# Kernel tuning notes

Hardware: AMD Instinct MI355X
Metric: run time of the kernel (lower is better)

Reference implementation:

```python
import jax, jax.numpy as jnp
import numpy as np

NUM_ORGAN = 13
EPS = 1e-05


def setup_inputs() -> dict:
    key = jax.random.key(0)
    k1, k2, k3 = jax.random.split(key, 3)
    B = 2
    pred_stage1 = jax.random.uniform(k1, (B, NUM_ORGAN + 1, 48, 256, 256), dtype=jnp.float32)
    pred_stage2 = jax.random.uniform(k2, (B, NUM_ORGAN + 1, 48, 256, 256), dtype=jnp.float32)
    target = jax.random.randint(k3, (B, 48, 256, 256), 0, NUM_ORGAN + 1, dtype=jnp.int32)
    return {"pred_stage1": pred_stage1, "pred_stage2": pred_stage2, "target": target}


def _dice_per_batch(pred, organ_target):
    # pred: (B, 14, D, H, W); organ_target: (B, 13, D, H, W) one-hot
    p = pred[:, 1:NUM_ORGAN + 1]                       # (B, 13, D, H, W)
    inter = jnp.sum(p * organ_target, axis=(2, 3, 4))  # (B, 13)
    p2 = jnp.sum(p * p, axis=(2, 3, 4))                # (B, 13)
    t2 = jnp.sum(organ_target, axis=(2, 3, 4))         # one-hot => t^2 == t
    dice = 2.0 * inter / (p2 + t2 + EPS)               # (B, 13)
    return jnp.sum(dice, axis=1) / NUM_ORGAN           # (B,)


def reference(pred_stage1, pred_stage2, target):
    organ_ids = jnp.arange(1, NUM_ORGAN + 1, dtype=target.dtype)
    # one-hot over organ classes 1..13 -> (B, 13, D, H, W)
    organ_target = (target[:, None] == organ_ids[None, :, None, None, None]).astype(pred_stage1.dtype)
    dice = _dice_per_batch(pred_stage1, organ_target) + _dice_per_batch(pred_stage2, organ_target)
    return jnp.mean(2.0 - dice)
```

## Files before the change

### kernel.cpp

```cpp
#include <hip/hip_runtime.h>

#define NORG 13
#define NCH  14
#define VOX  (48 * 256 * 256)
#define EPSF 1e-5f
#define CHUNK 8192
#define NCHUNK (VOX / CHUNK)
#define ITER (CHUNK / 4 / 256)
#define COMBO_STRIDE 16

__device__ __forceinline__ float wave_reduce(float v) {
#pragma unroll
    for (int off = 32; off; off >>= 1) v += __shfl_xor(v, off, 64);
    return v;
}

__global__ __launch_bounds__(256) void dice_partial(
    const float* __restrict__ pred1, const float* __restrict__ pred2,
    const int* __restrict__ tgt, float* __restrict__ acc_out)
{
    const int b     = blockIdx.y;
    const int chunk = blockIdx.x;
    const size_t v0 = (size_t)chunk * CHUNK;

    __shared__ unsigned char t_lds[CHUNK];
    __shared__ float acc[NORG * 5];

    if (threadIdx.x < NORG * 5) acc[threadIdx.x] = 0.f;

    const int4* tb = (const int4*)(tgt + (size_t)b * VOX + v0);
    uchar4* tl4 = (uchar4*)t_lds;
#pragma unroll
    for (int i = 0; i < ITER; ++i) {
        const int4 t = tb[i * 256 + threadIdx.x];
        tl4[i * 256 + threadIdx.x] =
            make_uchar4((unsigned char)t.x, (unsigned char)t.y,
                        (unsigned char)t.z, (unsigned char)t.w);
    }
    __syncthreads();

    const uchar4* tl = (const uchar4*)t_lds;
    const int lane = threadIdx.x & 63;

    for (int o = 0; o < NORG; ++o) {
        const int ch = o + 1;
        const float4* p1 = (const float4*)(pred1 + ((size_t)b * NCH + ch) * VOX + v0);
        const float4* p2 = (const float4*)(pred2 + ((size_t)b * NCH + ch) * VOX + v0);

        float i1 = 0.f, s1 = 0.f, i2 = 0.f, s2 = 0.f, cn = 0.f;
#pragma unroll
        for (int i = 0; i < ITER; ++i) {
            const int idx = i * 256 + threadIdx.x;
            const uchar4 t = tl[idx];
            const float4 a = p1[idx];
            const float4 c = p2[idx];
            const float m0 = (t.x == ch) ? 1.f : 0.f;
            const float m1 = (t.y == ch) ? 1.f : 0.f;
            const float m2 = (t.z == ch) ? 1.f : 0.f;
            const float m3 = (t.w == ch) ? 1.f : 0.f;
            s1 += a.x * a.x + a.y * a.y + a.z * a.z + a.w * a.w;
            s2 += c.x * c.x + c.y * c.y + c.z * c.z + c.w * c.w;
            i1 += m0 * a.x + m1 * a.y + m2 * a.z + m3 * a.w;
            i2 += m0 * c.x + m1 * c.y + m2 * c.z + m3 * c.w;
            cn += (m0 + m1) + (m2 + m3);
        }

        float vals[5] = {i1, s1, i2, s2, cn};
#pragma unroll
        for (int s = 0; s < 5; ++s) {
            const float r = wave_reduce(vals[s]);
            if (lane == 0) atomicAdd(&acc[o * 5 + s], r);
        }
    }

    __syncthreads();
    if (threadIdx.x < NORG * 5) {
        const int o = threadIdx.x / 5;
        const int s = threadIdx.x % 5;
        atomicAdd(&acc_out[(b * NORG + o) * COMBO_STRIDE + s], acc[threadIdx.x]);
    }
}

__global__ void dice_final(const float* __restrict__ acc,
                           float* __restrict__ out, int B)
{
    if (threadIdx.x == 0 && blockIdx.x == 0) {
        float total = 0.f;
        for (int b = 0; b < B; ++b) {
            float d1 = 0.f, d2 = 0.f;
            for (int o = 0; o < NORG; ++o) {
                const float* a = acc + (b * NORG + o) * COMBO_STRIDE;
                const float t2 = a[4];
                d1 += 2.f * a[0] / (a[1] + t2 + EPSF);
                d2 += 2.f * a[2] / (a[3] + t2 + EPSF);
            }
            total += 2.f - (d1 + d2) / (float)NORG;
        }
        out[0] = total / (float)B;
    }
}

extern "C" void kernel_launch(void* const* d_in, const int* in_sizes, int n_in,
                              void* d_out, int out_size, void* d_ws, size_t ws_size,
                              hipStream_t stream)
{
    const float* p1  = (const float*)d_in[0];
    const float* p2  = (const float*)d_in[1];
    const int*   tgt = (const int*)d_in[2];
    float*       out = (float*)d_out;
    float*       acc = (float*)d_ws;

    const int B = in_sizes[2] / VOX;

    hipMemsetAsync(d_ws, 0, (size_t)B * NORG * COMBO_STRIDE * sizeof(float), stream);

    dim3 grid(NCHUNK, B);
    dice_partial<<<grid, 256, 0, stream>>>(p1, p2, tgt, acc);
    dice_final<<<1, 64, 0, stream>>>(acc, out, B);
}
```

Baseline: 135.6 us.

## Halve chunk size, replace shuffle/LDS atomics with staged reduction, replicate global accumulators

Halves the per-block chunk, which doubles the number of blocks. The full 64-lane shuffle reduction and shared-memory atomics are replaced by a 2-step shuffle that writes partials into a shared-memory array, which one thread per slot then sums serially. Global atomics are spread over four replicated accumulator sets chosen by block index to lower contention, and the final kernel sums the replicas. Each block now re-reads targets for half as many voxels, and the serial 64-term sum per slot adds latency at the end of each block.

```diff
diff --git a/kernel.cpp b/kernel.cpp
--- a/kernel.cpp
+++ b/kernel.cpp
@@ -4,16 +4,11 @@
 #define NCH  14
 #define VOX  (48 * 256 * 256)
 #define EPSF 1e-5f
-#define CHUNK 8192
+#define CHUNK 4096
 #define NCHUNK (VOX / CHUNK)
 #define ITER (CHUNK / 4 / 256)
 #define COMBO_STRIDE 16
-
-__device__ __forceinline__ float wave_reduce(float v) {
-#pragma unroll
-    for (int off = 32; off; off >>= 1) v += __shfl_xor(v, off, 64);
-    return v;
-}
+#define NREP 4
 
 __global__ __launch_bounds__(256) void dice_partial(
     const float* __restrict__ pred1, const float* __restrict__ pred2,
@@ -24,9 +19,7 @@
     const size_t v0 = (size_t)chunk * CHUNK;
 
     __shared__ unsigned char t_lds[CHUNK];
-    __shared__ float acc[NORG * 5];
-
-    if (threadIdx.x < NORG * 5) acc[threadIdx.x] = 0.f;
+    __shared__ float red[4][16][NORG * 5];
 
     const int4* tb = (const int4*)(tgt + (size_t)b * VOX + v0);
     uchar4* tl4 = (uchar4*)t_lds;
@@ -41,6 +34,7 @@
 
     const uchar4* tl = (const uchar4*)t_lds;
     const int lane = threadIdx.x & 63;
+    const int wid  = threadIdx.x >> 6;
 
     for (int o = 0; o < NORG; ++o) {
         const int ch = o + 1;
@@ -68,16 +62,26 @@
         float vals[5] = {i1, s1, i2, s2, cn};
 #pragma unroll
         for (int s = 0; s < 5; ++s) {
-            const float r = wave_reduce(vals[s]);
-            if (lane == 0) atomicAdd(&acc[o * 5 + s], r);
+            float r = vals[s];
+            r += __shfl_xor(r, 1, 64);
+            r += __shfl_xor(r, 2, 64);
+            if ((lane & 3) == 0) red[wid][lane >> 2][o * 5 + s] = r;
         }
     }
 
     __syncthreads();
     if (threadIdx.x < NORG * 5) {
-        const int o = threadIdx.x / 5;
-        const int s = threadIdx.x % 5;
-        atomicAdd(&acc_out[(b * NORG + o) * COMBO_STRIDE + s], acc[threadIdx.x]);
+        float s = 0.f;
+#pragma unroll
+        for (int w = 0; w < 4; ++w)
+#pragma unroll
+            for (int g = 0; g < 16; ++g)
+                s += red[w][g][threadIdx.x];
+        const int o  = threadIdx.x / 5;
+        const int sl = threadIdx.x % 5;
+        const int bo = b * NORG + o;
+        const int rep = blockIdx.x & (NREP - 1);
+        atomicAdd(&acc_out[(rep * 26 + bo) * COMBO_STRIDE + sl], s);
     }
 }
 
@@ -89,10 +93,14 @@
         for (int b = 0; b < B; ++b) {
             float d1 = 0.f, d2 = 0.f;
             for (int o = 0; o < NORG; ++o) {
-                const float* a = acc + (b * NORG + o) * COMBO_STRIDE;
-                const float t2 = a[4];
-                d1 += 2.f * a[0] / (a[1] + t2 + EPSF);
-                d2 += 2.f * a[2] / (a[3] + t2 + EPSF);
+                const int bo = b * NORG + o;
+                float a0 = 0.f, a1 = 0.f, a2 = 0.f, a3 = 0.f, a4 = 0.f;
+                for (int r = 0; r < NREP; ++r) {
+                    const float* a = acc + (r * 26 + bo) * COMBO_STRIDE;
+                    a0 += a[0]; a1 += a[1]; a2 += a[2]; a3 += a[3]; a4 += a[4];
+                }
+                d1 += 2.f * a0 / (a1 + a4 + EPSF);
+                d2 += 2.f * a2 / (a3 + a4 + EPSF);
             }
             total += 2.f - (d1 + d2) / (float)NORG;
         }
@@ -112,7 +120,8 @@
 
     const int B = in_sizes[2] / VOX;
 
-    hipMemsetAsync(d_ws, 0, (size_t)B * NORG * COMBO_STRIDE * sizeof(float), stream);
+    hipMemsetAsync(d_ws, 0,
+                   (size_t)NREP * 26 * COMBO_STRIDE * sizeof(float), stream);
 
     dim3 grid(NCHUNK, B);
     dice_partial<<<grid, 256, 0, stream>>>(p1, p2, tgt, acc);
```

Result: slower. 138.5 us (+2.2%).
